# Performance work log

Hardware: AMD Instinct MI355X
Metric: run time of the kernel (lower is better)

The kernel has to match this reference:

```python
import jax, jax.numpy as jnp
import numpy as np

N = 100000
IN_DIM = 128
HID = 256
OUT_DIM = 128
E = 600000


def setup_inputs() -> dict:
    key = jax.random.key(0)
    ks = jax.random.split(key, 10)
    x = jax.random.normal(ks[0], (N, IN_DIM), dtype=jnp.float32)
    edge_index = jax.random.randint(ks[1], (2, E), 0, N, dtype=jnp.int32)

    def lin(k, fan_in, fan_out):
        kw, kb = jax.random.split(k)
        bound = 1.0 / np.sqrt(fan_in)
        W = jax.random.uniform(kw, (fan_in, fan_out), minval=-bound, maxval=bound, dtype=jnp.float32)
        b = jax.random.uniform(kb, (fan_out,), minval=-bound, maxval=bound, dtype=jnp.float32)
        return W, b

    W1a, b1a = lin(ks[2], IN_DIM, HID)
    W1b, b1b = lin(ks[3], HID, HID)
    W2a, b2a = lin(ks[4], HID, HID)
    W2b, b2b = lin(ks[5], HID, OUT_DIM)
    return {"x": x, "edge_index": edge_index,
            "W1a": W1a, "b1a": b1a, "W1b": W1b, "b1b": b1b,
            "W2a": W2a, "b2a": b2a, "W2b": W2b, "b2b": b2b}


def _gin_conv(x, src, dst, Wa, ba, Wb, bb):
    # GINConv with eps=0: h = (1+eps)*x + sum_{j in N(i)} x_j, then 2-layer MLP
    agg = jax.ops.segment_sum(x[src], dst, num_segments=N)  # [N, F]
    h = x + agg
    h = jax.nn.relu(h @ Wa + ba)
    return h @ Wb + bb


def reference(x, edge_index, W1a, b1a, W1b, b1b, W2a, b2a, W2b, b2b):
    src, dst = edge_index[0], edge_index[1]
    h = jax.nn.relu(_gin_conv(x, src, dst, W1a, b1a, W1b, b1b))
    h = jax.nn.relu(_gin_conv(h, src, dst, W2a, b2a, W2b, b2b))
    return h
```

## Files before the change

### kernel.cpp

```cpp
#include <hip/hip_runtime.h>
#include <stdint.h>

#define N_NODES 100000
#define E_EDGES 600000
#define IN_F    128
#define HID_F   256
#define OUT_F   128
#define NB_SCAN 98

typedef unsigned short ushort_t;
typedef short  short8  __attribute__((ext_vector_type(8)));
typedef float  floatx4 __attribute__((ext_vector_type(4)));

__device__ __forceinline__ float bf2f(unsigned u16) {
    return __uint_as_float(u16 << 16);
}
__device__ __forceinline__ ushort_t f2bf(float f) {
    unsigned u = __float_as_uint(f);
    return (ushort_t)((u + 0x7fffu + ((u >> 16) & 1u)) >> 16);
}

__global__ void k_prep(const float* __restrict__ x, ushort_t* __restrict__ xbf,
                       const float* __restrict__ W1a, const float* __restrict__ W1b,
                       const float* __restrict__ W2a, const float* __restrict__ W2b,
                       ushort_t* __restrict__ WT1a, ushort_t* __restrict__ WT1b,
                       ushort_t* __restrict__ WT2a, ushort_t* __restrict__ WT2b,
                       int* __restrict__ cursor, ushort_t* __restrict__ P) {
    int t = blockIdx.x * 256 + threadIdx.x;
    if (t < N_NODES * IN_F / 2) {
        float2 v = ((const float2*)x)[t];
        ((unsigned*)xbf)[t] = (unsigned)f2bf(v.x) | ((unsigned)f2bf(v.y) << 16);
    }
    if (t < N_NODES) cursor[t] = 0;
    if (t < 128) ((unsigned*)(P + (size_t)N_NODES * HID_F))[t] = 0;
    if (t < 64)  ((unsigned*)(xbf + (size_t)N_NODES * IN_F))[t] = 0;
    if (t < 32768) {
        int k = t >> 8, n = t & 255;
        WT1a[n * 128 + k] = f2bf(W1a[t]);
    } else if (t < 98304) {
        int i = t - 32768, k = i >> 8, n = i & 255;
        WT1b[n * 256 + k] = f2bf(W1b[i]);
    } else if (t < 163840) {
        int i = t - 98304, k = i >> 8, n = i & 255;
        WT2a[n * 256 + k] = f2bf(W2a[i]);
    } else if (t < 196608) {
        int i = t - 163840, k = i >> 7, n = i & 127;
        WT2b[n * 256 + k] = f2bf(W2b[i]);
    }
}

__global__ void k_hist(const int* __restrict__ dst, int* __restrict__ deg) {
    int e = blockIdx.x * 256 + threadIdx.x;
    if (e < E_EDGES) atomicAdd(&deg[dst[e]], 1);
}

__global__ void k_scan1(const int* __restrict__ deg, int* __restrict__ row_ptr,
                        int* __restrict__ psum) {
    __shared__ int s[1024];
    int t = threadIdx.x, i = blockIdx.x * 1024 + t;
    int v = (i < N_NODES) ? deg[i] : 0;
    s[t] = v;
    __syncthreads();
    for (int off = 1; off < 1024; off <<= 1) {
        int u = (t >= off) ? s[t - off] : 0;
        __syncthreads();
        if (t >= off) s[t] += u;
        __syncthreads();
    }
    if (i < N_NODES) row_ptr[i] = s[t] - v;
    if (t == 1023) psum[blockIdx.x] = s[t];
}

__global__ void k_scan2(int* __restrict__ psum) {
    __shared__ int s[128];
    int t = threadIdx.x;
    int v = (t < NB_SCAN) ? psum[t] : 0;
    s[t] = v;
    __syncthreads();
    for (int off = 1; off < 128; off <<= 1) {
        int u = (t >= off) ? s[t - off] : 0;
        __syncthreads();
        if (t >= off) s[t] += u;
        __syncthreads();
    }
    if (t < NB_SCAN) psum[t] = s[t] - v;
}

__global__ void k_scan3(int* __restrict__ row_ptr, const int* __restrict__ psum,
                        int* __restrict__ cursor) {
    int i = blockIdx.x * 1024 + threadIdx.x;
    if (i < N_NODES) {
        int r = row_ptr[i] + psum[i >> 10];
        row_ptr[i] = r;
        cursor[i]  = r;
    }
    if (i == 0) row_ptr[N_NODES] = E_EDGES;
}

__global__ void k_fill(const int* __restrict__ src, const int* __restrict__ dst,
                       int* __restrict__ cursor, int* __restrict__ colidx) {
    int e = blockIdx.x * 256 + threadIdx.x;
    if (e < E_EDGES) {
        int pos = atomicAdd(&cursor[dst[e]], 1);
        colidx[pos] = src[e];
    }
}

__global__ void k_agg128(const ushort_t* __restrict__ Xbf, const int* __restrict__ row_ptr,
                         const int* __restrict__ colidx, ushort_t* __restrict__ Out) {
    int node = blockIdx.x * 4 + (threadIdx.x >> 6);
    int lane = threadIdx.x & 63;
    int q = lane >> 4, l4 = lane & 15;
    const uint4* xr = (const uint4*)Xbf;
    uint4 u = xr[(size_t)node * 16 + l4];
    float a0 = q ? 0.f : bf2f(u.x & 0xffffu);
    float a1 = q ? 0.f : bf2f(u.x >> 16);
    float a2 = q ? 0.f : bf2f(u.y & 0xffffu);
    float a3 = q ? 0.f : bf2f(u.y >> 16);
    float a4 = q ? 0.f : bf2f(u.z & 0xffffu);
    float a5 = q ? 0.f : bf2f(u.z >> 16);
    float a6 = q ? 0.f : bf2f(u.w & 0xffffu);
    float a7 = q ? 0.f : bf2f(u.w >> 16);
    int r0 = row_ptr[node], r1 = row_ptr[node + 1];
    for (int base = r0 + q; base < r1; base += 8) {
        int j0 = colidx[base];
        int j1 = colidx[min(base + 4, r1 - 1)];
        j1 = (base + 4 < r1) ? j1 : N_NODES;
        uint4 w0 = xr[(size_t)j0 * 16 + l4];
        uint4 w1 = xr[(size_t)j1 * 16 + l4];
        a0 += bf2f(w0.x & 0xffffu) + bf2f(w1.x & 0xffffu);
        a1 += bf2f(w0.x >> 16)     + bf2f(w1.x >> 16);
        a2 += bf2f(w0.y & 0xffffu) + bf2f(w1.y & 0xffffu);
        a3 += bf2f(w0.y >> 16)     + bf2f(w1.y >> 16);
        a4 += bf2f(w0.z & 0xffffu) + bf2f(w1.z & 0xffffu);
        a5 += bf2f(w0.z >> 16)     + bf2f(w1.z >> 16);
        a6 += bf2f(w0.w & 0xffffu) + bf2f(w1.w & 0xffffu);
        a7 += bf2f(w0.w >> 16)     + bf2f(w1.w >> 16);
    }
    a0 += __shfl_xor(a0, 16, 64); a0 += __shfl_xor(a0, 32, 64);
    a1 += __shfl_xor(a1, 16, 64); a1 += __shfl_xor(a1, 32, 64);
    a2 += __shfl_xor(a2, 16, 64); a2 += __shfl_xor(a2, 32, 64);
    a3 += __shfl_xor(a3, 16, 64); a3 += __shfl_xor(a3, 32, 64);
    a4 += __shfl_xor(a4, 16, 64); a4 += __shfl_xor(a4, 32, 64);
    a5 += __shfl_xor(a5, 16, 64); a5 += __shfl_xor(a5, 32, 64);
    a6 += __shfl_xor(a6, 16, 64); a6 += __shfl_xor(a6, 32, 64);
    a7 += __shfl_xor(a7, 16, 64); a7 += __shfl_xor(a7, 32, 64);
    if (q == 0) {
        uint4 o;
        o.x = (unsigned)f2bf(a0) | ((unsigned)f2bf(a1) << 16);
        o.y = (unsigned)f2bf(a2) | ((unsigned)f2bf(a3) << 16);
        o.z = (unsigned)f2bf(a4) | ((unsigned)f2bf(a5) << 16);
        o.w = (unsigned)f2bf(a6) | ((unsigned)f2bf(a7) << 16);
        ((uint4*)Out)[(size_t)node * 16 + l4] = o;
    }
}

__global__ void k_agg256(const ushort_t* __restrict__ X, const int* __restrict__ row_ptr,
                         const int* __restrict__ colidx, ushort_t* __restrict__ Out) {
    int node = blockIdx.x * 4 + (threadIdx.x >> 6);
    int lane = threadIdx.x & 63;
    int h = lane >> 5, l5 = lane & 31;
    const uint4* xr = (const uint4*)X;
    uint4 u = xr[(size_t)node * 32 + l5];
    float a0 = h ? 0.f : bf2f(u.x & 0xffffu);
    float a1 = h ? 0.f : bf2f(u.x >> 16);
    float a2 = h ? 0.f : bf2f(u.y & 0xffffu);
    float a3 = h ? 0.f : bf2f(u.y >> 16);
    float a4 = h ? 0.f : bf2f(u.z & 0xffffu);
    float a5 = h ? 0.f : bf2f(u.z >> 16);
    float a6 = h ? 0.f : bf2f(u.w & 0xffffu);
    float a7 = h ? 0.f : bf2f(u.w >> 16);
    int r0 = row_ptr[node], r1 = row_ptr[node + 1];
    for (int base = r0 + h; base < r1; base += 8) {
        int j0 = colidx[base];
        int j1 = colidx[min(base + 2, r1 - 1)];
        int j2 = colidx[min(base + 4, r1 - 1)];
        int j3 = colidx[min(base + 6, r1 - 1)];
        j1 = (base + 2 < r1) ? j1 : N_NODES;
        j2 = (base + 4 < r1) ? j2 : N_NODES;
        j3 = (base + 6 < r1) ? j3 : N_NODES;
        uint4 w0 = xr[(size_t)j0 * 32 + l5];
        uint4 w1 = xr[(size_t)j1 * 32 + l5];
        uint4 w2 = xr[(size_t)j2 * 32 + l5];
        uint4 w3 = xr[(size_t)j3 * 32 + l5];
        a0 += (bf2f(w0.x & 0xffffu) + bf2f(w1.x & 0xffffu)) +
              (bf2f(w2.x & 0xffffu) + bf2f(w3.x & 0xffffu));
        a1 += (bf2f(w0.x >> 16) + bf2f(w1.x >> 16)) +
              (bf2f(w2.x >> 16) + bf2f(w3.x >> 16));
        a2 += (bf2f(w0.y & 0xffffu) + bf2f(w1.y & 0xffffu)) +
              (bf2f(w2.y & 0xffffu) + bf2f(w3.y & 0xffffu));
        a3 += (bf2f(w0.y >> 16) + bf2f(w1.y >> 16)) +
              (bf2f(w2.y >> 16) + bf2f(w3.y >> 16));
        a4 += (bf2f(w0.z & 0xffffu) + bf2f(w1.z & 0xffffu)) +
              (bf2f(w2.z & 0xffffu) + bf2f(w3.z & 0xffffu));
        a5 += (bf2f(w0.z >> 16) + bf2f(w1.z >> 16)) +
              (bf2f(w2.z >> 16) + bf2f(w3.z >> 16));
        a6 += (bf2f(w0.w & 0xffffu) + bf2f(w1.w & 0xffffu)) +
              (bf2f(w2.w & 0xffffu) + bf2f(w3.w & 0xffffu));
        a7 += (bf2f(w0.w >> 16) + bf2f(w1.w >> 16)) +
              (bf2f(w2.w >> 16) + bf2f(w3.w >> 16));
    }
    a0 += __shfl_xor(a0, 32, 64);
    a1 += __shfl_xor(a1, 32, 64);
    a2 += __shfl_xor(a2, 32, 64);
    a3 += __shfl_xor(a3, 32, 64);
    a4 += __shfl_xor(a4, 32, 64);
    a5 += __shfl_xor(a5, 32, 64);
    a6 += __shfl_xor(a6, 32, 64);
    a7 += __shfl_xor(a7, 32, 64);
    if (h == 0) {
        uint4 o;
        o.x = (unsigned)f2bf(a0) | ((unsigned)f2bf(a1) << 16);
        o.y = (unsigned)f2bf(a2) | ((unsigned)f2bf(a3) << 16);
        o.z = (unsigned)f2bf(a4) | ((unsigned)f2bf(a5) << 16);
        o.w = (unsigned)f2bf(a6) | ((unsigned)f2bf(a7) << 16);
        ((uint4*)Out)[(size_t)node * 32 + l5] = o;
    }
}

template <int FIN, int FOUT, bool OUT_F32>
__global__ __launch_bounds__(512, 4) void gemm_relu(
    const ushort_t* __restrict__ Act, const ushort_t* __restrict__ WT,
    const float* __restrict__ bias, void* __restrict__ Out, int nRows)
{
    constexpr int CPR = FIN / 8;
    constexpr int KC  = FIN / 32;
    constexpr int KP  = KC / 2;
    __shared__ ushort_t wt[128 * FIN];

    const int tid  = threadIdx.x;
    const int slab = blockIdx.y * 128;

    {
        const ushort_t* wsrc = WT + (size_t)slab * FIN;
#pragma unroll
        for (int rr = 0; rr < (128 * CPR) / 512; ++rr) {
            int ci  = rr * 512 + tid;
            int n   = ci / CPR;
            int csw = ci % CPR;
            int cor = csw ^ (n & 15);
            const ushort_t* g = wsrc + (size_t)n * FIN + cor * 8;
            __builtin_amdgcn_global_load_lds(
                (const __attribute__((address_space(1))) unsigned*)g,
                (__attribute__((address_space(3))) unsigned*)&wt[ci * 8],
                16, 0, 0);
        }
    }

    const int wave = tid >> 6, lane = tid & 63;
    const int quad = lane >> 4, l15 = lane & 15;
    const int rowBase = blockIdx.x * 256 + wave * 32;

    int r0 = rowBase + l15;
    int r1 = r0 + 16;
    r0 = (r0 < nRows) ? r0 : (nRows - 1);
    r1 = (r1 < nRows) ? r1 : (nRows - 1);
    const ushort_t* a0p = Act + (size_t)r0 * FIN + quad * 8;
    const ushort_t* a1p = Act + (size_t)r1 * FIN + quad * 8;

    short8 af[2][2][2];
#pragma unroll
    for (int kc = 0; kc < 2; ++kc) {
        af[0][0][kc] = *(const short8*)(a0p + kc * 32);
        af[0][1][kc] = *(const short8*)(a1p + kc * 32);
    }

    floatx4 acc[2][8];
#pragma unroll
    for (int mt = 0; mt < 2; ++mt)
#pragma unroll
        for (int nt = 0; nt < 8; ++nt)
#pragma unroll
            for (int r = 0; r < 4; ++r) acc[mt][nt][r] = 0.f;

    __syncthreads();

#pragma unroll
    for (int p = 0; p < KP; ++p) {
        const int cb = p & 1, nb = cb ^ 1;
        if (p + 1 < KP) {
#pragma unroll
            for (int kc = 0; kc < 2; ++kc) {
                af[nb][0][kc] = *(const short8*)(a0p + ((p + 1) * 2 + kc) * 32);
                af[nb][1][kc] = *(const short8*)(a1p + ((p + 1) * 2 + kc) * 32);
            }
        }
#pragma unroll
        for (int kc = 0; kc < 2; ++kc) {
            int chunk = (p * 2 + kc) * 4 + quad;
#pragma unroll
            for (int nt = 0; nt < 8; ++nt) {
                int n = nt * 16 + l15;
                int csw = chunk ^ (n & 15);
                short8 bfr = *(const short8*)&wt[n * FIN + csw * 8];
                acc[0][nt] = __builtin_amdgcn_mfma_f32_16x16x32_bf16(af[cb][0][kc], bfr, acc[0][nt], 0, 0, 0);
                acc[1][nt] = __builtin_amdgcn_mfma_f32_16x16x32_bf16(af[cb][1][kc], bfr, acc[1][nt], 0, 0, 0);
            }
        }
    }

#pragma unroll
    for (int mt = 0; mt < 2; ++mt) {
#pragma unroll
        for (int nt = 0; nt < 8; ++nt) {
            int col = slab + nt * 16 + l15;
            float bv = bias[col];
#pragma unroll
            for (int r = 0; r < 4; ++r) {
                int row = rowBase + mt * 16 + quad * 4 + r;
                if (row < nRows) {
                    float v = fmaxf(acc[mt][nt][r] + bv, 0.f);
                    if (OUT_F32)
                        ((float*)Out)[(size_t)row * FOUT + col] = v;
                    else
                        ((ushort_t*)Out)[(size_t)row * FOUT + col] = f2bf(v);
                }
            }
        }
    }
}

extern "C" void kernel_launch(void* const* d_in, const int* in_sizes, int n_in,
                              void* d_out, int out_size, void* d_ws, size_t ws_size,
                              hipStream_t stream) {
    const float* x   = (const float*)d_in[0];
    const int*   ei  = (const int*)d_in[1];
    const int*   src = ei;
    const int*   dst = ei + E_EDGES;
    const float* W1a = (const float*)d_in[2];
    const float* b1a = (const float*)d_in[3];
    const float* W1b = (const float*)d_in[4];
    const float* b1b = (const float*)d_in[5];
    const float* W2a = (const float*)d_in[6];
    const float* b2a = (const float*)d_in[7];
    const float* W2b = (const float*)d_in[8];
    const float* b2b = (const float*)d_in[9];

    const size_t NP1 = N_NODES + 1;
    ushort_t* P       = (ushort_t*)d_ws;
    ushort_t* Q       = P + NP1 * HID_F;
    ushort_t* xbf     = Q;
    int*      row_ptr = (int*)(Q + NP1 * HID_F);
    int*      cursor  = row_ptr + (N_NODES + 4);
    int*      colidx  = cursor + N_NODES;
    int*      psum    = colidx + E_EDGES;
    ushort_t* WT1a    = (ushort_t*)(psum + 128);
    ushort_t* WT1b    = WT1a + 256 * 128;
    ushort_t* WT2a    = WT1b + 256 * 256;
    ushort_t* WT2b    = WT2a + 256 * 256;

    k_prep<<<(N_NODES * IN_F / 2 + 255) / 256, 256, 0, stream>>>(
        x, xbf, W1a, W1b, W2a, W2b, WT1a, WT1b, WT2a, WT2b, cursor, P);

    k_hist <<<(E_EDGES + 255) / 256, 256, 0, stream>>>(dst, cursor);
    k_scan1<<<NB_SCAN, 1024, 0, stream>>>(cursor, row_ptr, psum);
    k_scan2<<<1, 128, 0, stream>>>(psum);
    k_scan3<<<NB_SCAN, 1024, 0, stream>>>(row_ptr, psum, cursor);
    k_fill <<<(E_EDGES + 255) / 256, 256, 0, stream>>>(src, dst, cursor, colidx);

    const int ROWB = (N_NODES + 255) / 256;

    k_agg128<<<N_NODES / 4, 256, 0, stream>>>(xbf, row_ptr, colidx, P);
    gemm_relu<128, 256, false><<<dim3(ROWB, 2), 512, 0, stream>>>(P, WT1a, b1a, Q, N_NODES);
    gemm_relu<256, 256, false><<<dim3(ROWB, 2), 512, 0, stream>>>(Q, WT1b, b1b, P, N_NODES);

    k_agg256<<<N_NODES / 4, 256, 0, stream>>>(P, row_ptr, colidx, Q);
    gemm_relu<256, 256, false><<<dim3(ROWB, 2), 512, 0, stream>>>(Q, WT2a, b2a, P, N_NODES);
    gemm_relu<256, 128, true><<<dim3(ROWB, 1), 512, 0, stream>>>(P, WT2b, b2b, d_out, N_NODES);
}
```

Baseline: 393.3 us.

## Fuse each two-layer MLP into one kernel keeping the hidden tile in LDS

Replaces the four separate GEMM+ReLU launches with two fused MLP kernels. Each block computes the first layer for 128 rows across all 256 hidden columns, stores the bf16 hidden activations in swizzled shared memory, then runs the second layer from LDS. This removes the global-memory write and re-read of the intermediate hidden activations and two kernel launches. Weights are now read directly from global/L2 per MFMA instead of being staged in LDS. Each wave now holds 16 accumulators over 16 rows, which raises register pressure.

```diff
diff --git a/kernel.cpp b/kernel.cpp
--- a/kernel.cpp
+++ b/kernel.cpp
@@ -25,14 +25,14 @@
                        const float* __restrict__ W2a, const float* __restrict__ W2b,
                        ushort_t* __restrict__ WT1a, ushort_t* __restrict__ WT1b,
                        ushort_t* __restrict__ WT2a, ushort_t* __restrict__ WT2b,
-                       int* __restrict__ cursor, ushort_t* __restrict__ P) {
+                       int* __restrict__ cursor, ushort_t* __restrict__ Q) {
     int t = blockIdx.x * 256 + threadIdx.x;
     if (t < N_NODES * IN_F / 2) {
         float2 v = ((const float2*)x)[t];
         ((unsigned*)xbf)[t] = (unsigned)f2bf(v.x) | ((unsigned)f2bf(v.y) << 16);
     }
     if (t < N_NODES) cursor[t] = 0;
-    if (t < 128) ((unsigned*)(P + (size_t)N_NODES * HID_F))[t] = 0;
+    if (t < 128) ((unsigned*)(Q + (size_t)N_NODES * HID_F))[t] = 0;
     if (t < 64)  ((unsigned*)(xbf + (size_t)N_NODES * IN_F))[t] = 0;
     if (t < 32768) {
         int k = t >> 8, n = t & 255;
@@ -219,102 +219,92 @@
 }
 
 template <int FIN, int FOUT, bool OUT_F32>
-__global__ __launch_bounds__(512, 4) void gemm_relu(
-    const ushort_t* __restrict__ Act, const ushort_t* __restrict__ WT,
-    const float* __restrict__ bias, void* __restrict__ Out, int nRows)
+__global__ __launch_bounds__(512, 4) void mlp2(
+    const ushort_t* __restrict__ Act,
+    const ushort_t* __restrict__ WTa, const float* __restrict__ ba,
+    const ushort_t* __restrict__ WTb, const float* __restrict__ bb,
+    void* __restrict__ Out, int nRows)
 {
-    constexpr int CPR = FIN / 8;
-    constexpr int KC  = FIN / 32;
-    constexpr int KP  = KC / 2;
-    __shared__ ushort_t wt[128 * FIN];
+    constexpr int KC1 = FIN / 32;
+    constexpr int NT2 = FOUT / 16;
+    __shared__ ushort_t T[128 * 256];
 
     const int tid  = threadIdx.x;
-    const int slab = blockIdx.y * 128;
-
-    {
-        const ushort_t* wsrc = WT + (size_t)slab * FIN;
-#pragma unroll
-        for (int rr = 0; rr < (128 * CPR) / 512; ++rr) {
-            int ci  = rr * 512 + tid;
-            int n   = ci / CPR;
-            int csw = ci % CPR;
-            int cor = csw ^ (n & 15);
-            const ushort_t* g = wsrc + (size_t)n * FIN + cor * 8;
-            __builtin_amdgcn_global_load_lds(
-                (const __attribute__((address_space(1))) unsigned*)g,
-                (__attribute__((address_space(3))) unsigned*)&wt[ci * 8],
-                16, 0, 0);
-        }
-    }
-
     const int wave = tid >> 6, lane = tid & 63;
     const int quad = lane >> 4, l15 = lane & 15;
-    const int rowBase = blockIdx.x * 256 + wave * 32;
+    const int rowBase = blockIdx.x * 128 + wave * 16;
 
     int r0 = rowBase + l15;
-    int r1 = r0 + 16;
     r0 = (r0 < nRows) ? r0 : (nRows - 1);
-    r1 = (r1 < nRows) ? r1 : (nRows - 1);
-    const ushort_t* a0p = Act + (size_t)r0 * FIN + quad * 8;
-    const ushort_t* a1p = Act + (size_t)r1 * FIN + quad * 8;
-
-    short8 af[2][2][2];
-#pragma unroll
-    for (int kc = 0; kc < 2; ++kc) {
-        af[0][0][kc] = *(const short8*)(a0p + kc * 32);
-        af[0][1][kc] = *(const short8*)(a1p + kc * 32);
-    }
-
-    floatx4 acc[2][8];
-#pragma unroll
-    for (int mt = 0; mt < 2; ++mt)
-#pragma unroll
-        for (int nt = 0; nt < 8; ++nt)
-#pragma unroll
-            for (int r = 0; r < 4; ++r) acc[mt][nt][r] = 0.f;
-
+    const ushort_t* ap = Act + (size_t)r0 * FIN + quad * 8;
+
+    short8 af[KC1];
+#pragma unroll
+    for (int kc = 0; kc < KC1; ++kc) af[kc] = *(const short8*)(ap + kc * 32);
+
+    floatx4 acc[16];
+#pragma unroll
+    for (int nt = 0; nt < 16; ++nt)
+#pragma unroll
+        for (int r = 0; r < 4; ++r) acc[nt][r] = 0.f;
+
+#pragma unroll
+    for (int kc = 0; kc < KC1; ++kc) {
+#pragma unroll
+        for (int nt = 0; nt < 16; ++nt) {
+            int n = nt * 16 + l15;
+            short8 bfr = *(const short8*)(WTa + (size_t)n * FIN + kc * 32 + quad * 8);
+            acc[nt] = __builtin_amdgcn_mfma_f32_16x16x32_bf16(af[kc], bfr, acc[nt], 0, 0, 0);
+        }
+    }
+
+#pragma unroll
+    for (int nt = 0; nt < 16; ++nt) {
+        int col = nt * 16 + l15;
+        float bv = ba[col];
+        int g = col >> 3;
+#pragma unroll
+        for (int r = 0; r < 4; ++r) {
+            int row = wave * 16 + quad * 4 + r;
+            float v = fmaxf(acc[nt][r] + bv, 0.f);
+            int gs = g ^ (row & 7);
+            T[row * 256 + gs * 8 + (col & 7)] = f2bf(v);
+        }
+    }
     __syncthreads();
 
 #pragma unroll
-    for (int p = 0; p < KP; ++p) {
-        const int cb = p & 1, nb = cb ^ 1;
-        if (p + 1 < KP) {
-#pragma unroll
-            for (int kc = 0; kc < 2; ++kc) {
-                af[nb][0][kc] = *(const short8*)(a0p + ((p + 1) * 2 + kc) * 32);
-                af[nb][1][kc] = *(const short8*)(a1p + ((p + 1) * 2 + kc) * 32);
-            }
+    for (int nt = 0; nt < NT2; ++nt)
+#pragma unroll
+        for (int r = 0; r < 4; ++r) acc[nt][r] = 0.f;
+
+    const int trow = wave * 16 + l15;
+#pragma unroll
+    for (int kc = 0; kc < 8; ++kc) {
+        int g  = kc * 4 + quad;
+        int gs = g ^ (trow & 7);
+        short8 af2 = *(const short8*)&T[trow * 256 + gs * 8];
+#pragma unroll
+        for (int nt = 0; nt < NT2; ++nt) {
+            int n = nt * 16 + l15;
+            short8 bfr = *(const short8*)(WTb + (size_t)n * 256 + kc * 32 + quad * 8);
+            acc[nt] = __builtin_amdgcn_mfma_f32_16x16x32_bf16(af2, bfr, acc[nt], 0, 0, 0);
         }
-#pragma unroll
-        for (int kc = 0; kc < 2; ++kc) {
-            int chunk = (p * 2 + kc) * 4 + quad;
-#pragma unroll
-            for (int nt = 0; nt < 8; ++nt) {
-                int n = nt * 16 + l15;
-                int csw = chunk ^ (n & 15);
-                short8 bfr = *(const short8*)&wt[n * FIN + csw * 8];
-                acc[0][nt] = __builtin_amdgcn_mfma_f32_16x16x32_bf16(af[cb][0][kc], bfr, acc[0][nt], 0, 0, 0);
-                acc[1][nt] = __builtin_amdgcn_mfma_f32_16x16x32_bf16(af[cb][1][kc], bfr, acc[1][nt], 0, 0, 0);
-            }
-        }
-    }
-
-#pragma unroll
-    for (int mt = 0; mt < 2; ++mt) {
-#pragma unroll
-        for (int nt = 0; nt < 8; ++nt) {
-            int col = slab + nt * 16 + l15;
-            float bv = bias[col];
-#pragma unroll
-            for (int r = 0; r < 4; ++r) {
-                int row = rowBase + mt * 16 + quad * 4 + r;
-                if (row < nRows) {
-                    float v = fmaxf(acc[mt][nt][r] + bv, 0.f);
-                    if (OUT_F32)
-                        ((float*)Out)[(size_t)row * FOUT + col] = v;
-                    else
-                        ((ushort_t*)Out)[(size_t)row * FOUT + col] = f2bf(v);
-                }
+    }
+
+#pragma unroll
+    for (int nt = 0; nt < NT2; ++nt) {
+        int col = nt * 16 + l15;
+        float bv = bb[col];
+#pragma unroll
+        for (int r = 0; r < 4; ++r) {
+            int row = rowBase + quad * 4 + r;
+            if (row < nRows) {
+                float v = fmaxf(acc[nt][r] + bv, 0.f);
+                if (OUT_F32)
+                    ((float*)Out)[(size_t)row * FOUT + col] = v;
+                else
+                    ((ushort_t*)Out)[(size_t)row * FOUT + col] = f2bf(v);
             }
         }
     }
@@ -350,7 +340,7 @@
     ushort_t* WT2b    = WT2a + 256 * 256;
 
     k_prep<<<(N_NODES * IN_F / 2 + 255) / 256, 256, 0, stream>>>(
-        x, xbf, W1a, W1b, W2a, W2b, WT1a, WT1b, WT2a, WT2b, cursor, P);
+        x, xbf, W1a, W1b, W2a, W2b, WT1a, WT1b, WT2a, WT2b, cursor, Q);
 
     k_hist <<<(E_EDGES + 255) / 256, 256, 0, stream>>>(dst, cursor);
     k_scan1<<<NB_SCAN, 1024, 0, stream>>>(cursor, row_ptr, psum);
@@ -358,13 +348,11 @@
     k_scan3<<<NB_SCAN, 1024, 0, stream>>>(row_ptr, psum, cursor);
     k_fill <<<(E_EDGES + 255) / 256, 256, 0, stream>>>(src, dst, cursor, colidx);
 
-    const int ROWB = (N_NODES + 255) / 256;
+    const int RB = (N_NODES + 127) / 128;
 
     k_agg128<<<N_NODES / 4, 256, 0, stream>>>(xbf, row_ptr, colidx, P);
-    gemm_relu<128, 256, false><<<dim3(ROWB, 2), 512, 0, stream>>>(P, WT1a, b1a, Q, N_NODES);
-    gemm_relu<256, 256, false><<<dim3(ROWB, 2), 512, 0, stream>>>(Q, WT1b, b1b, P, N_NODES);
-
-    k_agg256<<<N_NODES / 4, 256, 0, stream>>>(P, row_ptr, colidx, Q);
-    gemm_relu<256, 256, false><<<dim3(ROWB, 2), 512, 0, stream>>>(Q, WT2a, b2a, P, N_NODES);
-    gemm_relu<256, 128, true><<<dim3(ROWB, 1), 512, 0, stream>>>(P, WT2b, b2b, d_out, N_NODES);
-}
+    mlp2<128, 256, false><<<RB, 512, 0, stream>>>(P, WT1a, b1a, WT1b, b1b, Q, N_NODES);
+
+    k_agg256<<<N_NODES / 4, 256, 0, stream>>>(Q, row_ptr, colidx, P);
+    mlp2<256, 128, true><<<RB, 512, 0, stream>>>(P, WT2a, b2a, WT2b, b2b, d_out, N_NODES);
+}
```

Result: slower. 669.3 us (+70.2%).

## Halve GEMM row tile per block and preload all A fragments up front

Applied to the files above, without the earlier changes.

The GEMM kernel now gives each wave 16 rows instead of 32, so each block covers 128 rows and the grid has twice as many row blocks. All A-operand fragments for the full K dimension are loaded into registers before the weight slab is staged into LDS, which replaces the double-buffered prefetch. The aim is more blocks for better load balance and overlap of the global A loads with the LDS weight fill. The cost is that each weight fragment read from LDS now feeds one MFMA instead of two, and the weight slab is loaded into LDS by twice as many blocks.

```diff
diff --git a/kernel.cpp b/kernel.cpp
--- a/kernel.cpp
+++ b/kernel.cpp
@@ -225,11 +225,22 @@
 {
     constexpr int CPR = FIN / 8;
     constexpr int KC  = FIN / 32;
-    constexpr int KP  = KC / 2;
     __shared__ ushort_t wt[128 * FIN];
 
     const int tid  = threadIdx.x;
     const int slab = blockIdx.y * 128;
+    const int wave = tid >> 6, lane = tid & 63;
+    const int quad = lane >> 4, l15 = lane & 15;
+    const int rowBase = blockIdx.x * 128 + wave * 16;
+
+    int r0 = rowBase + l15;
+    r0 = (r0 < nRows) ? r0 : (nRows - 1);
+    const ushort_t* ap = Act + (size_t)r0 * FIN + quad * 8;
+
+    short8 af[KC];
+#pragma unroll
+    for (int kc = 0; kc < KC; ++kc)
+        af[kc] = *(const short8*)(ap + kc * 32);
 
     {
         const ushort_t* wsrc = WT + (size_t)slab * FIN;
@@ -247,74 +258,39 @@
         }
     }
 
-    const int wave = tid >> 6, lane = tid & 63;
-    const int quad = lane >> 4, l15 = lane & 15;
-    const int rowBase = blockIdx.x * 256 + wave * 32;
-
-    int r0 = rowBase + l15;
-    int r1 = r0 + 16;
-    r0 = (r0 < nRows) ? r0 : (nRows - 1);
-    r1 = (r1 < nRows) ? r1 : (nRows - 1);
-    const ushort_t* a0p = Act + (size_t)r0 * FIN + quad * 8;
-    const ushort_t* a1p = Act + (size_t)r1 * FIN + quad * 8;
-
-    short8 af[2][2][2];
-#pragma unroll
-    for (int kc = 0; kc < 2; ++kc) {
-        af[0][0][kc] = *(const short8*)(a0p + kc * 32);
-        af[0][1][kc] = *(const short8*)(a1p + kc * 32);
-    }
-
-    floatx4 acc[2][8];
-#pragma unroll
-    for (int mt = 0; mt < 2; ++mt)
-#pragma unroll
-        for (int nt = 0; nt < 8; ++nt)
-#pragma unroll
-            for (int r = 0; r < 4; ++r) acc[mt][nt][r] = 0.f;
+    floatx4 acc[8];
+#pragma unroll
+    for (int nt = 0; nt < 8; ++nt)
+#pragma unroll
+        for (int r = 0; r < 4; ++r) acc[nt][r] = 0.f;
 
     __syncthreads();
 
 #pragma unroll
-    for (int p = 0; p < KP; ++p) {
-        const int cb = p & 1, nb = cb ^ 1;
-        if (p + 1 < KP) {
-#pragma unroll
-            for (int kc = 0; kc < 2; ++kc) {
-                af[nb][0][kc] = *(const short8*)(a0p + ((p + 1) * 2 + kc) * 32);
-                af[nb][1][kc] = *(const short8*)(a1p + ((p + 1) * 2 + kc) * 32);
-            }
+    for (int kc = 0; kc < KC; ++kc) {
+        int chunk = kc * 4 + quad;
+#pragma unroll
+        for (int nt = 0; nt < 8; ++nt) {
+            int n = nt * 16 + l15;
+            int csw = chunk ^ (n & 15);
+            short8 bfr = *(const short8*)&wt[n * FIN + csw * 8];
+            acc[nt] = __builtin_amdgcn_mfma_f32_16x16x32_bf16(af[kc], bfr, acc[nt], 0, 0, 0);
         }
-#pragma unroll
-        for (int kc = 0; kc < 2; ++kc) {
-            int chunk = (p * 2 + kc) * 4 + quad;
-#pragma unroll
-            for (int nt = 0; nt < 8; ++nt) {
-                int n = nt * 16 + l15;
-                int csw = chunk ^ (n & 15);
-                short8 bfr = *(const short8*)&wt[n * FIN + csw * 8];
-                acc[0][nt] = __builtin_amdgcn_mfma_f32_16x16x32_bf16(af[cb][0][kc], bfr, acc[0][nt], 0, 0, 0);
-                acc[1][nt] = __builtin_amdgcn_mfma_f32_16x16x32_bf16(af[cb][1][kc], bfr, acc[1][nt], 0, 0, 0);
-            }
-        }
-    }
-
-#pragma unroll
-    for (int mt = 0; mt < 2; ++mt) {
-#pragma unroll
-        for (int nt = 0; nt < 8; ++nt) {
-            int col = slab + nt * 16 + l15;
-            float bv = bias[col];
-#pragma unroll
-            for (int r = 0; r < 4; ++r) {
-                int row = rowBase + mt * 16 + quad * 4 + r;
-                if (row < nRows) {
-                    float v = fmaxf(acc[mt][nt][r] + bv, 0.f);
-                    if (OUT_F32)
-                        ((float*)Out)[(size_t)row * FOUT + col] = v;
-                    else
-                        ((ushort_t*)Out)[(size_t)row * FOUT + col] = f2bf(v);
-                }
+    }
+
+#pragma unroll
+    for (int nt = 0; nt < 8; ++nt) {
+        int col = slab + nt * 16 + l15;
+        float bv = bias[col];
+#pragma unroll
+        for (int r = 0; r < 4; ++r) {
+            int row = rowBase + quad * 4 + r;
+            if (row < nRows) {
+                float v = fmaxf(acc[nt][r] + bv, 0.f);
+                if (OUT_F32)
+                    ((float*)Out)[(size_t)row * FOUT + col] = v;
+                else
+                    ((ushort_t*)Out)[(size_t)row * FOUT + col] = f2bf(v);
             }
         }
     }
@@ -358,13 +334,13 @@
     k_scan3<<<NB_SCAN, 1024, 0, stream>>>(row_ptr, psum, cursor);
     k_fill <<<(E_EDGES + 255) / 256, 256, 0, stream>>>(src, dst, cursor, colidx);
 
-    const int ROWB = (N_NODES + 255) / 256;
+    const int RB = (N_NODES + 127) / 128;
 
     k_agg128<<<N_NODES / 4, 256, 0, stream>>>(xbf, row_ptr, colidx, P);
-    gemm_relu<128, 256, false><<<dim3(ROWB, 2), 512, 0, stream>>>(P, WT1a, b1a, Q, N_NODES);
-    gemm_relu<256, 256, false><<<dim3(ROWB, 2), 512, 0, stream>>>(Q, WT1b, b1b, P, N_NODES);
+    gemm_relu<128, 256, false><<<dim3(RB, 2), 512, 0, stream>>>(P, WT1a, b1a, Q, N_NODES);
+    gemm_relu<256, 256, false><<<dim3(RB, 2), 512, 0, stream>>>(Q, WT1b, b1b, P, N_NODES);
 
     k_agg256<<<N_NODES / 4, 256, 0, stream>>>(P, row_ptr, colidx, Q);
-    gemm_relu<256, 256, false><<<dim3(ROWB, 2), 512, 0, stream>>>(Q, WT2a, b2a, P, N_NODES);
-    gemm_relu<256, 128, true><<<dim3(ROWB, 1), 512, 0, stream>>>(P, WT2b, b2b, d_out, N_NODES);
-}
+    gemm_relu<256, 256, false><<<dim3(RB, 2), 512, 0, stream>>>(Q, WT2a, b2a, P, N_NODES);
+    gemm_relu<256, 128, true><<<dim3(RB, 1), 512, 0, stream>>>(P, WT2b, b2b, d_out, N_NODES);
+}
```

New measurement: 419.0 us. 6.5% more time.

## Make GEMM kernels persistent so each block loads weights once and loops over row tiles

Applied to the files above, without the earlier changes.

Replaces the grid of one block per 256-row tile with a fixed grid of 256 row-workers (512 blocks for the 256-wide outputs, two column slabs each). Each block loads its weight slab into LDS once and then strides over row tiles, which removes the repeated weight loads and LDS fills the old grid did for every tile. The block index is remapped so the two slabs of the same row tile run in neighbouring blocks, which helps share activation reads in L2. The trade-off is fewer blocks and less latency hiding from oversubscription, plus possible imbalance across the 391 tiles.

```diff
diff --git a/kernel.cpp b/kernel.cpp
--- a/kernel.cpp
+++ b/kernel.cpp
@@ -228,8 +228,20 @@
     constexpr int KP  = KC / 2;
     __shared__ ushort_t wt[128 * FIN];
 
-    const int tid  = threadIdx.x;
-    const int slab = blockIdx.y * 128;
+    const int tid = threadIdx.x;
+    const int bid = blockIdx.x;
+
+    int p, sl;
+    if (FOUT == 256) {
+        const int group = bid >> 4, w = bid & 15;
+        p  = group * 8 + (w & 7);
+        sl = w >> 3;
+    } else {
+        p  = bid;
+        sl = 0;
+    }
+    const int slab   = sl * 128;
+    const int nTiles = (nRows + 255) / 256;
 
     {
         const ushort_t* wsrc = WT + (size_t)slab * FIN;
@@ -249,71 +261,74 @@
 
     const int wave = tid >> 6, lane = tid & 63;
     const int quad = lane >> 4, l15 = lane & 15;
-    const int rowBase = blockIdx.x * 256 + wave * 32;
-
-    int r0 = rowBase + l15;
-    int r1 = r0 + 16;
-    r0 = (r0 < nRows) ? r0 : (nRows - 1);
-    r1 = (r1 < nRows) ? r1 : (nRows - 1);
-    const ushort_t* a0p = Act + (size_t)r0 * FIN + quad * 8;
-    const ushort_t* a1p = Act + (size_t)r1 * FIN + quad * 8;
-
-    short8 af[2][2][2];
-#pragma unroll
-    for (int kc = 0; kc < 2; ++kc) {
-        af[0][0][kc] = *(const short8*)(a0p + kc * 32);
-        af[0][1][kc] = *(const short8*)(a1p + kc * 32);
-    }
-
-    floatx4 acc[2][8];
-#pragma unroll
-    for (int mt = 0; mt < 2; ++mt)
-#pragma unroll
-        for (int nt = 0; nt < 8; ++nt)
-#pragma unroll
-            for (int r = 0; r < 4; ++r) acc[mt][nt][r] = 0.f;
 
     __syncthreads();
 
-#pragma unroll
-    for (int p = 0; p < KP; ++p) {
-        const int cb = p & 1, nb = cb ^ 1;
-        if (p + 1 < KP) {
+    for (int t = p; t < nTiles; t += 256) {
+        const int rowBase = t * 256 + wave * 32;
+
+        int r0 = rowBase + l15;
+        int r1 = r0 + 16;
+        r0 = (r0 < nRows) ? r0 : (nRows - 1);
+        r1 = (r1 < nRows) ? r1 : (nRows - 1);
+        const ushort_t* a0p = Act + (size_t)r0 * FIN + quad * 8;
+        const ushort_t* a1p = Act + (size_t)r1 * FIN + quad * 8;
+
+        short8 af[2][2][2];
+#pragma unroll
+        for (int kc = 0; kc < 2; ++kc) {
+            af[0][0][kc] = *(const short8*)(a0p + kc * 32);
+            af[0][1][kc] = *(const short8*)(a1p + kc * 32);
+        }
+
+        floatx4 acc[2][8];
+#pragma unroll
+        for (int mt = 0; mt < 2; ++mt)
+#pragma unroll
+            for (int nt = 0; nt < 8; ++nt)
+#pragma unroll
+                for (int r = 0; r < 4; ++r) acc[mt][nt][r] = 0.f;
+
+#pragma unroll
+        for (int pp = 0; pp < KP; ++pp) {
+            const int cb = pp & 1, nb = cb ^ 1;
+            if (pp + 1 < KP) {
+#pragma unroll
+                for (int kc = 0; kc < 2; ++kc) {
+                    af[nb][0][kc] = *(const short8*)(a0p + ((pp + 1) * 2 + kc) * 32);
+                    af[nb][1][kc] = *(const short8*)(a1p + ((pp + 1) * 2 + kc) * 32);
+                }
+            }
 #pragma unroll
             for (int kc = 0; kc < 2; ++kc) {
-                af[nb][0][kc] = *(const short8*)(a0p + ((p + 1) * 2 + kc) * 32);
-                af[nb][1][kc] = *(const short8*)(a1p + ((p + 1) * 2 + kc) * 32);
+                int chunk = (pp * 2 + kc) * 4 + quad;
+#pragma unroll
+                for (int nt = 0; nt < 8; ++nt) {
+                    int n = nt * 16 + l15;
+                    int csw = chunk ^ (n & 15);
+                    short8 bfr = *(const short8*)&wt[n * FIN + csw * 8];
+                    acc[0][nt] = __builtin_amdgcn_mfma_f32_16x16x32_bf16(af[cb][0][kc], bfr, acc[0][nt], 0, 0, 0);
+                    acc[1][nt] = __builtin_amdgcn_mfma_f32_16x16x32_bf16(af[cb][1][kc], bfr, acc[1][nt], 0, 0, 0);
+                }
             }
         }
-#pragma unroll
-        for (int kc = 0; kc < 2; ++kc) {
-            int chunk = (p * 2 + kc) * 4 + quad;
+
+#pragma unroll
+        for (int mt = 0; mt < 2; ++mt) {
 #pragma unroll
             for (int nt = 0; nt < 8; ++nt) {
-                int n = nt * 16 + l15;
-                int csw = chunk ^ (n & 15);
-                short8 bfr = *(const short8*)&wt[n * FIN + csw * 8];
-                acc[0][nt] = __builtin_amdgcn_mfma_f32_16x16x32_bf16(af[cb][0][kc], bfr, acc[0][nt], 0, 0, 0);
-                acc[1][nt] = __builtin_amdgcn_mfma_f32_16x16x32_bf16(af[cb][1][kc], bfr, acc[1][nt], 0, 0, 0);
-            }
-        }
-    }
-
-#pragma unroll
-    for (int mt = 0; mt < 2; ++mt) {
-#pragma unroll
-        for (int nt = 0; nt < 8; ++nt) {
-            int col = slab + nt * 16 + l15;
-            float bv = bias[col];
-#pragma unroll
-            for (int r = 0; r < 4; ++r) {
-                int row = rowBase + mt * 16 + quad * 4 + r;
-                if (row < nRows) {
-                    float v = fmaxf(acc[mt][nt][r] + bv, 0.f);
-                    if (OUT_F32)
-                        ((float*)Out)[(size_t)row * FOUT + col] = v;
-                    else
-                        ((ushort_t*)Out)[(size_t)row * FOUT + col] = f2bf(v);
+                int col = slab + nt * 16 + l15;
+                float bv = bias[col];
+#pragma unroll
+                for (int r = 0; r < 4; ++r) {
+                    int row = rowBase + mt * 16 + quad * 4 + r;
+                    if (row < nRows) {
+                        float v = fmaxf(acc[mt][nt][r] + bv, 0.f);
+                        if (OUT_F32)
+                            ((float*)Out)[(size_t)row * FOUT + col] = v;
+                        else
+                            ((ushort_t*)Out)[(size_t)row * FOUT + col] = f2bf(v);
+                    }
                 }
             }
         }
@@ -358,13 +373,11 @@
     k_scan3<<<NB_SCAN, 1024, 0, stream>>>(row_ptr, psum, cursor);
     k_fill <<<(E_EDGES + 255) / 256, 256, 0, stream>>>(src, dst, cursor, colidx);
 
-    const int ROWB = (N_NODES + 255) / 256;
-
     k_agg128<<<N_NODES / 4, 256, 0, stream>>>(xbf, row_ptr, colidx, P);
-    gemm_relu<128, 256, false><<<dim3(ROWB, 2), 512, 0, stream>>>(P, WT1a, b1a, Q, N_NODES);
-    gemm_relu<256, 256, false><<<dim3(ROWB, 2), 512, 0, stream>>>(Q, WT1b, b1b, P, N_NODES);
+    gemm_relu<128, 256, false><<<512, 512, 0, stream>>>(P, WT1a, b1a, Q, N_NODES);
+    gemm_relu<256, 256, false><<<512, 512, 0, stream>>>(Q, WT1b, b1b, P, N_NODES);
 
     k_agg256<<<N_NODES / 4, 256, 0, stream>>>(P, row_ptr, colidx, Q);
-    gemm_relu<256, 256, false><<<dim3(ROWB, 2), 512, 0, stream>>>(Q, WT2a, b2a, P, N_NODES);
-    gemm_relu<256, 128, true><<<dim3(ROWB, 1), 512, 0, stream>>>(P, WT2b, b2b, d_out, N_NODES);
-}
+    gemm_relu<256, 256, false><<<512, 512, 0, stream>>>(Q, WT2a, b2a, P, N_NODES);
+    gemm_relu<256, 128, true><<<256, 512, 0, stream>>>(P, WT2b, b2b, d_out, N_NODES);
+}
```

Result: slower. 858.6 us (+118.3%).
